# Kernel optimization log

Hardware: AMD Instinct MI355X
Metric: run time of the kernel (lower is better)

Reference implementation:

```python
import jax, jax.numpy as jnp
import numpy as np

N, E = 50000, 500000
G_DIM, H1, H2 = 256, 128, 128
N_REL, N_BASES = 8, 30  # 2 * n_speakers**2 with n_speakers=2


def setup_inputs() -> dict:
    key = jax.random.key(0)
    ks = jax.random.split(key, 12)
    inp = {
        "node_features": jax.random.normal(ks[0], (N, G_DIM), jnp.float32),
        "edge_index": jax.random.randint(ks[1], (2, E), 0, N, jnp.int64),
        "edge_norm": jax.random.uniform(ks[2], (E,), jnp.float32),
        "edge_type": jax.random.randint(ks[3], (E,), 0, N_REL, jnp.int64),
        # RGCNConv (basis decomposition) params
        "basis": jax.random.normal(ks[4], (N_BASES, G_DIM, H1), jnp.float32) / np.sqrt(G_DIM),
        "comp": jax.random.normal(ks[5], (N_REL, N_BASES), jnp.float32) / np.sqrt(N_BASES),
        "root": jax.random.normal(ks[6], (G_DIM, H1), jnp.float32) / np.sqrt(G_DIM),
        "bias1": jnp.zeros((H1,), jnp.float32),
        # GATv2Conv params (heads=1)
        "w_l": jax.random.normal(ks[7], (H1, H2), jnp.float32) / np.sqrt(H1),
        "w_r": jax.random.normal(ks[8], (H1, H2), jnp.float32) / np.sqrt(H1),
        "att": jax.random.normal(ks[9], (H2,), jnp.float32) / np.sqrt(H2),
        "bias2": jnp.zeros((H2,), jnp.float32),
    }
    return inp


def reference(node_features, edge_index, edge_norm, edge_type,
              basis, comp, root, bias1, w_l, w_r, att, bias2):
    # NOTE: edge_norm is accepted but unused, matching the original forward.
    src, dst = edge_index[0], edge_index[1]
    n = node_features.shape[0]
    R = comp.shape[0]

    # ---- RGCNConv with basis decomposition, per-relation mean aggregation ----
    Wr = jnp.einsum('rb,bio->rio', comp, basis)            # [R, g_dim, h1]
    xr = jnp.einsum('ni,rio->nro', node_features, Wr)      # [N, R, h1]
    msg = xr[src, edge_type]                               # [E, h1] gather per edge
    seg = dst * R + edge_type                              # segment = (node, relation)
    sums = jax.ops.segment_sum(msg, seg, num_segments=n * R)
    cnts = jax.ops.segment_sum(jnp.ones((msg.shape[0],), msg.dtype), seg, num_segments=n * R)
    mean = sums / jnp.maximum(cnts, 1.0)[:, None]          # per-(node,relation) mean
    agg = mean.reshape(n, R, -1).sum(axis=1)               # sum over relations
    x1 = agg + node_features @ root + bias1                # [N, h1]

    # ---- GATv2Conv (heads=1, add_self_loops=True) ----
    loop = jnp.arange(n, dtype=src.dtype)
    s2 = jnp.concatenate([src, loop])
    d2 = jnp.concatenate([dst, loop])
    xl = x1 @ w_l                                          # source transform [N, h2]
    xrt = x1 @ w_r                                         # target transform [N, h2]
    e = jax.nn.leaky_relu(xl[s2] + xrt[d2], 0.2) @ att     # [E+N] edge scores
    emax = jax.ops.segment_max(e, d2, num_segments=n)      # self-loops => every seg nonempty
    ex = jnp.exp(e - emax[d2])
    denom = jax.ops.segment_sum(ex, d2, num_segments=n)
    alpha = ex / denom[d2]                                 # segment softmax over incoming edges
    out = jax.ops.segment_sum(alpha[:, None] * xl[s2], d2, num_segments=n) + bias2
    return out
```

## Files before the change

kernel.cpp:

```cpp
#include <hip/hip_runtime.h>
#include <hip/hip_bf16.h>
#include <cstdint>
#include <cstddef>

#define NN 50000
#define NE 500000
#define GD 256
#define H1 128
#define H2 128
#define NREL 8
#define NBASES 30
#define XRLD (NREL * H1)
#define NCHUNKS ((NN + 1023) / 1024)

typedef __attribute__((ext_vector_type(8))) short bf16x8;
typedef __attribute__((ext_vector_type(4))) float f32x4;
typedef __attribute__((ext_vector_type(8))) unsigned short u16x8;
typedef __attribute__((ext_vector_type(4))) unsigned int u32x4;

__device__ __forceinline__ float lrelu(float x) { return x > 0.f ? x : 0.2f * x; }

__device__ __forceinline__ unsigned short f2bf(float x) {
  union { float f; uint32_t u; } v; v.f = x;
  uint32_t r = v.u + 0x7FFF + ((v.u >> 16) & 1);
  return (unsigned short)(r >> 16);
}
__device__ __forceinline__ float bf2f(unsigned short u) {
  union { uint32_t u; float f; } v; v.u = ((uint32_t)u) << 16;
  return v.f;
}

template <int N>
__device__ __forceinline__ void wait_vmcnt() {
  asm volatile("s_waitcnt vmcnt(%0)" :: "n"(N) : "memory");
}

__device__ __forceinline__ void gload_lds(const unsigned short* gp, unsigned short* lp) {
  __builtin_amdgcn_global_load_lds(
      (const __attribute__((address_space(1))) void*)gp,
      (__attribute__((address_space(3))) void*)lp, 16, 0, 0);
}

__global__ void k_cast(const float* __restrict__ in, unsigned short* __restrict__ out) {
  int i = blockIdx.x * 256 + threadIdx.x;
  const float4* p = (const float4*)(in + (size_t)i * 8);
  float4 a = p[0], b = p[1];
  u16x8 r;
  r[0] = f2bf(a.x); r[1] = f2bf(a.y); r[2] = f2bf(a.z); r[3] = f2bf(a.w);
  r[4] = f2bf(b.x); r[5] = f2bf(b.y); r[6] = f2bf(b.z); r[7] = f2bf(b.w);
  *(u16x8*)(out + (size_t)i * 8) = r;
}

__global__ void k_wr(const float* __restrict__ basis, const float* __restrict__ comp,
                     unsigned short* __restrict__ wrb_t) {
  int idx = blockIdx.x * 256 + threadIdx.x;
  int n = idx >> 8;
  int k = idx & 255;
  int r = n >> 7, o = n & 127;
  float acc = 0.f;
  #pragma unroll
  for (int b = 0; b < NBASES; b++)
    acc += comp[r * NBASES + b] * basis[((size_t)b * GD + k) * H1 + o];
  wrb_t[idx] = f2bf(acc);
}

__global__ __launch_bounds__(256)
void k_prep2(const float* __restrict__ root, const float* __restrict__ w_l,
             const float* __restrict__ w_r, const float* __restrict__ bias1,
             unsigned short* __restrict__ btf, float* __restrict__ biasv) {
  __shared__ float wcol[128];
  __shared__ float red[128];
  int c = blockIdx.x;
  int t = threadIdx.x;
  if (t < 128) {
    float v = (c < H2) ? w_l[t * H2 + c] : w_r[t * H2 + (c - H2)];
    wcol[t] = v;
    btf[c * 384 + t] = f2bf(v);
  }
  __syncthreads();
  const float4* rp = (const float4*)(root + (size_t)t * H1);
  float acc = 0.f;
  #pragma unroll
  for (int j4 = 0; j4 < 32; j4++) {
    float4 r4 = rp[j4];
    acc += r4.x * wcol[j4 * 4 + 0] + r4.y * wcol[j4 * 4 + 1] +
           r4.z * wcol[j4 * 4 + 2] + r4.w * wcol[j4 * 4 + 3];
  }
  btf[c * 384 + 128 + t] = f2bf(acc);
  if (t < 128) red[t] = bias1[t] * wcol[t];
  __syncthreads();
  for (int st = 64; st > 0; st >>= 1) {
    if (t < st) red[t] += red[t + st];
    __syncthreads();
  }
  if (t == 0) biasv[c] = red[0];
}

template <int K, int WM>
__global__ __launch_bounds__(256, 3)
void k_mgemm(const unsigned short* __restrict__ A, const unsigned short* __restrict__ Bt,
             unsigned short* __restrict__ C, int M, int N, int gx) {
  constexpr int BM = WM * 32;
  constexpr int ACH = BM * 4;
  constexpr int TCH = ACH + 512;
  constexpr int LPT = TCH / 256;
  constexpr int NS = K / 32;
  constexpr int ABUF = BM * 32;
  constexpr int BBUF = 128 * 32;
  extern __shared__ unsigned short lds[];
  const int tid = threadIdx.x;
  const int lane = tid & 63;
  const int wave = tid >> 6;

  const int nwg = gridDim.x;
  const int q = nwg >> 3, r = nwg & 7;
  const int xcd = blockIdx.x & 7, bi = blockIdx.x >> 3;
  const int wg = (xcd < r ? xcd * (q + 1) : r * (q + 1) + (xcd - r) * q) + bi;
  const int bx = wg % gx;
  const int by = wg / gx;
  const int row0 = by * BM;
  const int colb = bx * 128;
  const int wcol = (wave & 1) * 64;
  const int wrow = (wave >> 1) * (WM * 16);
  const int lr = lane & 15;
  const int lko = lane >> 4;

  f32x4 acc[WM][4];
  #pragma unroll
  for (int i = 0; i < WM; i++)
    #pragma unroll
    for (int j = 0; j < 4; j++) acc[i][j] = (f32x4){0.f, 0.f, 0.f, 0.f};

  auto stage = [&](int k0, int b) {
    unsigned short* as = lds + b * ABUF;
    unsigned short* bs = lds + 3 * ABUF + b * BBUF;
    #pragma unroll
    for (int it = 0; it < LPT; it++) {
      int ci = it * 256 + tid;
      if (ci < ACH) {
        int row = ci >> 2, cs = ci & 3;
        int s = (row & 3) ^ ((row >> 2) & 3);
        int gm = row0 + row; if (gm >= M) gm = M - 1;
        gload_lds(A + (size_t)gm * K + k0 + ((cs ^ s) << 3), as + (size_t)ci * 8);
      } else {
        int cj = ci - ACH;
        int row = cj >> 2, cs = cj & 3;
        int s = (row & 3) ^ ((row >> 2) & 3);
        gload_lds(Bt + (size_t)(colb + row) * K + k0 + ((cs ^ s) << 3), bs + (size_t)cj * 8);
      }
    }
  };

  auto compute = [&](int b) {
    const unsigned short* as = lds + b * ABUF;
    const unsigned short* bs = lds + 3 * ABUF + b * BBUF;
    bf16x8 af[WM], bfr[4];
    #pragma unroll
    for (int mb = 0; mb < WM; mb++) {
      int rowL = wrow + mb * 16 + lr;
      int s = (rowL & 3) ^ ((rowL >> 2) & 3);
      af[mb] = *(const bf16x8*)&as[rowL * 32 + ((lko ^ s) << 3)];
    }
    #pragma unroll
    for (int nb = 0; nb < 4; nb++) {
      int colL = wcol + nb * 16 + lr;
      int s = (colL & 3) ^ ((colL >> 2) & 3);
      bfr[nb] = *(const bf16x8*)&bs[colL * 32 + ((lko ^ s) << 3)];
    }
    #pragma unroll
    for (int mb = 0; mb < WM; mb++)
      #pragma unroll
      for (int nb = 0; nb < 4; nb++)
        acc[mb][nb] = __builtin_amdgcn_mfma_f32_16x16x32_bf16(af[mb], bfr[nb], acc[mb][nb], 0, 0, 0);
  };

  stage(0, 0);
  stage(32, 1);
  wait_vmcnt<LPT>();
  __builtin_amdgcn_sched_barrier(0);
  __builtin_amdgcn_s_barrier();
  #pragma unroll
  for (int s = 0; s < NS; s++) {
    if (s + 2 < NS) stage((s + 2) * 32, (s + 2) % 3);
    compute(s % 3);
    if (s + 1 < NS) {
      if (s + 2 < NS) wait_vmcnt<LPT>();
      else            wait_vmcnt<0>();
      __builtin_amdgcn_sched_barrier(0);
      __builtin_amdgcn_s_barrier();
    }
  }

  __syncthreads();
  unsigned short* Cs = lds;
  const int orow = lko * 4;
  #pragma unroll
  for (int mb = 0; mb < WM; mb++) {
    #pragma unroll
    for (int i = 0; i < 4; i++) {
      int row = wrow + mb * 16 + orow + i;
      int sw = (row & 7) << 3;
      #pragma unroll
      for (int nb = 0; nb < 4; nb++) {
        int col = wcol + nb * 16 + lr;
        Cs[row * 128 + (col ^ sw)] = f2bf(acc[mb][nb][i]);
      }
    }
  }
  __syncthreads();
  #pragma unroll
  for (int it = 0; it < BM / 16; it++) {
    int off = it * 256 + tid;
    int row = off >> 4, jb = off & 15;
    int grow = row0 + row;
    if (grow < M) {
      int idx = row * 128 + ((jb * 8) ^ ((row & 7) << 3));
      u32x4 val = *(const u32x4*)&Cs[idx];
      __builtin_nontemporal_store(val, (u32x4*)&C[(size_t)grow * N + colb + jb * 8]);
    }
  }
}

__global__ __launch_bounds__(256, 3)
void k_fused(const unsigned short* __restrict__ A1, const unsigned short* __restrict__ A2,
             const unsigned short* __restrict__ Bt, const float* __restrict__ biasv,
             unsigned short* __restrict__ xl, unsigned short* __restrict__ xrt, int M) {
  constexpr int K = 384, NS = 12, LPT = 4;
  extern __shared__ unsigned short lds[];
  const int tid = threadIdx.x;
  const int lane = tid & 63;
  const int wave = tid >> 6;

  const int nwg = gridDim.x;
  const int q = nwg >> 3, r = nwg & 7;
  const int xcd = blockIdx.x & 7, bi = blockIdx.x >> 3;
  const int wg = (xcd < r ? xcd * (q + 1) : r * (q + 1) + (xcd - r) * q) + bi;
  const int bx = wg & 1;
  const int by = wg >> 1;
  const int row0 = by * 128;
  const int colb = bx * 128;
  const int wcol = (wave & 1) * 64;
  const int wrow = (wave >> 1) * 64;
  const int lr = lane & 15;
  const int lko = lane >> 4;

  f32x4 acc[4][4];
  #pragma unroll
  for (int i = 0; i < 4; i++)
    #pragma unroll
    for (int j = 0; j < 4; j++) acc[i][j] = (f32x4){0.f, 0.f, 0.f, 0.f};

  auto stage = [&](int k0, int b) {
    unsigned short* as = lds + b * 4096;
    unsigned short* bs = lds + 3 * 4096 + b * 4096;
    #pragma unroll
    for (int it = 0; it < LPT; it++) {
      int ci = it * 256 + tid;
      if (ci < 512) {
        int row = ci >> 2, cs = ci & 3;
        int s = (row & 3) ^ ((row >> 2) & 3);
        int gm = row0 + row; if (gm >= M) gm = M - 1;
        const unsigned short* gp;
        if (k0 < 128) gp = A1 + (size_t)gm * 128 + k0 + ((cs ^ s) << 3);
        else          gp = A2 + (size_t)gm * 256 + (k0 - 128) + ((cs ^ s) << 3);
        gload_lds(gp, as + (size_t)ci * 8);
      } else {
        int cj = ci - 512;
        int row = cj >> 2, cs = cj & 3;
        int s = (row & 3) ^ ((row >> 2) & 3);
        gload_lds(Bt + (size_t)(colb + row) * K + k0 + ((cs ^ s) << 3), bs + (size_t)cj * 8);
      }
    }
  };

  auto compute = [&](int b) {
    const unsigned short* as = lds + b * 4096;
    const unsigned short* bs = lds + 3 * 4096 + b * 4096;
    bf16x8 af[4], bfr[4];
    #pragma unroll
    for (int mb = 0; mb < 4; mb++) {
      int rowL = wrow + mb * 16 + lr;
      int s = (rowL & 3) ^ ((rowL >> 2) & 3);
      af[mb] = *(const bf16x8*)&as[rowL * 32 + ((lko ^ s) << 3)];
    }
    #pragma unroll
    for (int nb = 0; nb < 4; nb++) {
      int colL = wcol + nb * 16 + lr;
      int s = (colL & 3) ^ ((colL >> 2) & 3);
      bfr[nb] = *(const bf16x8*)&bs[colL * 32 + ((lko ^ s) << 3)];
    }
    #pragma unroll
    for (int mb = 0; mb < 4; mb++)
      #pragma unroll
      for (int nb = 0; nb < 4; nb++)
        acc[mb][nb] = __builtin_amdgcn_mfma_f32_16x16x32_bf16(af[mb], bfr[nb], acc[mb][nb], 0, 0, 0);
  };

  stage(0, 0);
  stage(32, 1);
  wait_vmcnt<LPT>();
  __builtin_amdgcn_sched_barrier(0);
  __builtin_amdgcn_s_barrier();
  #pragma unroll
  for (int s = 0; s < NS; s++) {
    if (s + 2 < NS) stage((s + 2) * 32, (s + 2) % 3);
    compute(s % 3);
    if (s + 1 < NS) {
      if (s + 2 < NS) wait_vmcnt<LPT>();
      else            wait_vmcnt<0>();
      __builtin_amdgcn_sched_barrier(0);
      __builtin_amdgcn_s_barrier();
    }
  }

  __syncthreads();
  unsigned short* Cs = lds;
  const int orow = lko * 4;
  #pragma unroll
  for (int mb = 0; mb < 4; mb++) {
    #pragma unroll
    for (int i = 0; i < 4; i++) {
      int row = wrow + mb * 16 + orow + i;
      int sw = (row & 7) << 3;
      #pragma unroll
      for (int nb = 0; nb < 4; nb++) {
        int col = wcol + nb * 16 + lr;
        Cs[row * 128 + (col ^ sw)] = f2bf(acc[mb][nb][i] + biasv[colb + col]);
      }
    }
  }
  __syncthreads();
  unsigned short* Cout = bx ? xrt : xl;
  #pragma unroll
  for (int it = 0; it < 8; it++) {
    int off = it * 256 + tid;
    int row = off >> 4, jb = off & 15;
    int grow = row0 + row;
    if (grow < M) {
      int idx = row * 128 + ((jb * 8) ^ ((row & 7) << 3));
      *(u16x8*)&Cout[(size_t)grow * 128 + jb * 8] = *(const u16x8*)&Cs[idx];
    }
  }
}

__global__ void k_deg(const int* __restrict__ ei, const int* __restrict__ et,
                      int* __restrict__ cnt2) {
  int e = blockIdx.x * 256 + threadIdx.x;
  if (e < NE) atomicAdd(&cnt2[ei[NE + e] * NREL + et[e]], 1);
}

__device__ __forceinline__ int node_deg(const int* cnt2, int n) {
  const int4* p = (const int4*)(cnt2 + n * NREL);
  int4 a = p[0], b = p[1];
  return a.x + a.y + a.z + a.w + b.x + b.y + b.z + b.w;
}

__global__ void k_scan_a(const int* __restrict__ cnt2, int* __restrict__ parts) {
  __shared__ int lds[256];
  int t = threadIdx.x;
  int base = blockIdx.x * 1024 + t * 4;
  int s = 0;
  #pragma unroll
  for (int j = 0; j < 4; j++) s += (base + j < NN) ? node_deg(cnt2, base + j) : 0;
  lds[t] = s;
  __syncthreads();
  for (int st = 128; st > 0; st >>= 1) {
    if (t < st) lds[t] += lds[t + st];
    __syncthreads();
  }
  if (t == 0) parts[blockIdx.x] = lds[0];
}

__global__ void k_scan_b(int* __restrict__ parts) {
  int t = threadIdx.x;
  int v = (t < NCHUNKS) ? parts[t] : 0;
  int x = v;
  #pragma unroll
  for (int off = 1; off < 64; off <<= 1) {
    int y = __shfl_up(x, off, 64);
    if (t >= off) x += y;
  }
  if (t < NCHUNKS) parts[t] = x - v;
}

__global__ void k_scan_c(const int* __restrict__ cnt2, const int* __restrict__ parts,
                         int* __restrict__ rowptr) {
  __shared__ int lds[256];
  int t = threadIdx.x;
  int base = blockIdx.x * 1024 + t * 4;
  int v[4];
  int s = 0;
  #pragma unroll
  for (int j = 0; j < 4; j++) { v[j] = (base + j < NN) ? node_deg(cnt2, base + j) : 0; s += v[j]; }
  lds[t] = s;
  __syncthreads();
  for (int st = 1; st < 256; st <<= 1) {
    int add = (t >= st) ? lds[t - st] : 0;
    __syncthreads();
    lds[t] += add;
    __syncthreads();
  }
  int excl = lds[t] - s;
  int off = parts[blockIdx.x];
  int run = 0;
  #pragma unroll
  for (int j = 0; j < 4; j++) {
    run += v[j];
    if (base + j < NN) rowptr[base + j + 1] = off + excl + run;
  }
  if (blockIdx.x == 0 && t == 0) rowptr[0] = 0;
}

__global__ void k_scatter(const int* __restrict__ ei, const int* __restrict__ et,
                          const int* __restrict__ rowptr, const int* __restrict__ cnt2,
                          int* __restrict__ cursor, int* __restrict__ csr,
                          float* __restrict__ wgt) {
  int e = blockIdx.x * 256 + threadIdx.x;
  if (e < NE) {
    int d = ei[NE + e];
    int r = et[e];
    int pos = atomicAdd(&cursor[d], 1);
    int slot = rowptr[d] + pos;
    csr[slot] = ei[e] | (r << 20);
    wgt[slot] = 1.0f / (float)cnt2[d * NREL + r];
  }
}

__global__ __launch_bounds__(256)
void k_rgcn(const unsigned short* __restrict__ xr, const int* __restrict__ csr2,
            const float* __restrict__ wgt, const int* __restrict__ rowptr,
            unsigned short* __restrict__ agg) {
  int wpair = (blockIdx.x * 256 + threadIdx.x) >> 6;
  int lane = threadIdx.x & 63;
  int hb = lane & 32;
  int l = lane & 31;
  int wid = wpair * 2 + (hb >> 5);
  if (wid >= NN) return;
  int c0 = l * 4;
  float a0 = 0.f, a1 = 0.f, a2 = 0.f, a3 = 0.f;
  int beg = rowptr[wid], end = rowptr[wid + 1];
  for (int j0 = beg; j0 < end; j0 += 32) {
    int nv = end - j0; if (nv > 32) nv = 32;
    int pk = (l < nv) ? csr2[j0 + l] : 0;
    float wk = (l < nv) ? wgt[j0 + l] : 0.f;
    for (int t = 0; t < nv; t += 8) {
      uint2 wv[8]; float wz[8];
      #pragma unroll
      for (int z = 0; z < 8; z++) {
        int p = __shfl(pk, hb + t + z, 64);
        wz[z] = __shfl(wk, hb + t + z, 64);
        if (t + z < nv) {
          size_t off = (size_t)(p & 0xFFFFF) * XRLD + (p >> 20) * H1 + c0;
          wv[z] = *(const uint2*)(xr + off);
        } else {
          wv[z] = make_uint2(0, 0);
        }
      }
      #pragma unroll
      for (int z = 0; z < 8; z++) {
        a0 += wz[z] * bf2f((unsigned short)(wv[z].x & 0xffff));
        a1 += wz[z] * bf2f((unsigned short)(wv[z].x >> 16));
        a2 += wz[z] * bf2f((unsigned short)(wv[z].y & 0xffff));
        a3 += wz[z] * bf2f((unsigned short)(wv[z].y >> 16));
      }
    }
  }
  uint2 packed;
  packed.x = (uint32_t)f2bf(a0) | ((uint32_t)f2bf(a1) << 16);
  packed.y = (uint32_t)f2bf(a2) | ((uint32_t)f2bf(a3) << 16);
  *(uint2*)&agg[(size_t)wid * H1 + c0] = packed;
}

__global__ __launch_bounds__(256)
void k_gat(const unsigned short* __restrict__ xl, const unsigned short* __restrict__ xrt,
           const int* __restrict__ csr2, const int* __restrict__ rowptr,
           const float* __restrict__ att, const float* __restrict__ bias2,
           float* __restrict__ out) {
  int wpair = (blockIdx.x * 256 + threadIdx.x) >> 6;
  int lane = threadIdx.x & 63;
  int hb = lane & 32;
  int l = lane & 31;
  int wid = wpair * 2 + (hb >> 5);
  if (wid >= NN) return;
  int c0 = l * 4;
  float4 at = *(const float4*)(att + c0);
  uint2 wr2 = *(const uint2*)(xrt + (size_t)wid * 128 + c0);
  float xr0 = bf2f((unsigned short)(wr2.x & 0xffff));
  float xr1 = bf2f((unsigned short)(wr2.x >> 16));
  float xr2 = bf2f((unsigned short)(wr2.y & 0xffff));
  float xr3 = bf2f((unsigned short)(wr2.y >> 16));
  uint2 wv0 = *(const uint2*)(xl + (size_t)wid * 128 + c0);
  float v0 = bf2f((unsigned short)(wv0.x & 0xffff));
  float v1 = bf2f((unsigned short)(wv0.x >> 16));
  float v2 = bf2f((unsigned short)(wv0.y & 0xffff));
  float v3 = bf2f((unsigned short)(wv0.y >> 16));
  float ep = lrelu(v0 + xr0) * at.x + lrelu(v1 + xr1) * at.y +
             lrelu(v2 + xr2) * at.z + lrelu(v3 + xr3) * at.w;
  #pragma unroll
  for (int off = 16; off > 0; off >>= 1) ep += __shfl_xor(ep, off, 64);
  float m = ep, s = 1.f, o0 = v0, o1 = v1, o2 = v2, o3 = v3;
  int beg = rowptr[wid], end = rowptr[wid + 1];
  for (int j0 = beg; j0 < end; j0 += 32) {
    int nv = end - j0; if (nv > 32) nv = 32;
    int pk = (l < nv) ? csr2[j0 + l] : 0;
    for (int t = 0; t < nv; t += 8) {
      float u0[8], u1[8], u2[8], u3[8], p[8];
      #pragma unroll
      for (int z = 0; z < 8; z++) {
        int src = __shfl(pk, hb + t + z, 64) & 0xFFFFF;
        uint2 wu;
        if (t + z < nv) wu = *(const uint2*)(xl + (size_t)src * 128 + c0);
        else            wu = make_uint2(0, 0);
        u0[z] = bf2f((unsigned short)(wu.x & 0xffff));
        u1[z] = bf2f((unsigned short)(wu.x >> 16));
        u2[z] = bf2f((unsigned short)(wu.y & 0xffff));
        u3[z] = bf2f((unsigned short)(wu.y >> 16));
      }
      #pragma unroll
      for (int z = 0; z < 8; z++)
        p[z] = lrelu(u0[z] + xr0) * at.x + lrelu(u1[z] + xr1) * at.y +
               lrelu(u2[z] + xr2) * at.z + lrelu(u3[z] + xr3) * at.w;
      #pragma unroll
      for (int off = 16; off > 0; off >>= 1) {
        #pragma unroll
        for (int z = 0; z < 8; z++) p[z] += __shfl_xor(p[z], off, 64);
      }
      #pragma unroll
      for (int z = 0; z < 8; z++) if (t + z >= nv) p[z] = -1e30f;
      float pm = p[0];
      #pragma unroll
      for (int z = 1; z < 8; z++) pm = fmaxf(pm, p[z]);
      float mn = fmaxf(m, pm);
      float sc = __expf(m - mn);
      float e[8];
      #pragma unroll
      for (int z = 0; z < 8; z++) e[z] = __expf(p[z] - mn);
      float es = 0.f, e0 = 0.f, e1 = 0.f, e2 = 0.f, e3 = 0.f;
      #pragma unroll
      for (int z = 0; z < 8; z++) {
        es += e[z]; e0 += e[z] * u0[z]; e1 += e[z] * u1[z];
        e2 += e[z] * u2[z]; e3 += e[z] * u3[z];
      }
      s = s * sc + es;
      o0 = o0 * sc + e0; o1 = o1 * sc + e1;
      o2 = o2 * sc + e2; o3 = o3 * sc + e3;
      m = mn;
    }
  }
  float inv = 1.f / s;
  float4 b2 = *(const float4*)(bias2 + c0);
  float4 res = make_float4(o0 * inv + b2.x, o1 * inv + b2.y,
                           o2 * inv + b2.z, o3 * inv + b2.w);
  *(float4*)&out[(size_t)wid * H1 + c0] = res;
}

extern "C" void kernel_launch(void* const* d_in, const int* in_sizes, int n_in,
                              void* d_out, int out_size, void* d_ws, size_t ws_size,
                              hipStream_t stream) {
  const float* nf    = (const float*)d_in[0];
  const int*   ei    = (const int*)d_in[1];
  const int*   et    = (const int*)d_in[3];
  const float* basis = (const float*)d_in[4];
  const float* comp  = (const float*)d_in[5];
  const float* root  = (const float*)d_in[6];
  const float* bias1 = (const float*)d_in[7];
  const float* w_l   = (const float*)d_in[8];
  const float* w_r   = (const float*)d_in[9];
  const float* att   = (const float*)d_in[10];
  const float* bias2 = (const float*)d_in[11];
  float* out = (float*)d_out;

  char* ws = (char*)d_ws;
  unsigned short* xr_bf  = (unsigned short*)ws;
  unsigned short* nf_bf  = (unsigned short*)(ws + 102400000);
  unsigned short* wrb_t  = (unsigned short*)(ws + 128000000);
  unsigned short* btf    = (unsigned short*)(ws + 128524288);
  float*          biasv  = (float*)(ws + 128720896);
  unsigned short* agg_bf = (unsigned short*)(ws + 128721920);
  int*            cursor = (int*)(ws + 141521920);
  int*            cnt2   = cursor + NN;
  int*            rowptr = cnt2 + NN * NREL;
  int*            csr    = rowptr + NN + 1;
  int*            parts  = csr + NE;
  float*          wgt    = (float*)(parts + 64);
  unsigned short* xl_bf  = (unsigned short*)ws;
  unsigned short* xrt_bf = (unsigned short*)(ws + 12800000);

  hipMemsetAsync(cursor, 0, (1 + NREL) * NN * sizeof(int), stream);

  k_cast<<<(NN * GD / 8) / 256, 256, 0, stream>>>(nf, nf_bf);
  k_wr<<<(XRLD * GD) / 256, 256, 0, stream>>>(basis, comp, wrb_t);
  k_prep2<<<256, 256, 0, stream>>>(root, w_l, w_r, bias1, btf, biasv);

  const int GY128 = (NN + 127) / 128;
  k_mgemm<256, 4><<<8 * GY128, 256, 49152, stream>>>(
      nf_bf, wrb_t, xr_bf, NN, XRLD, 8);

  k_deg<<<(NE + 255) / 256, 256, 0, stream>>>(ei, et, cnt2);
  k_scan_a<<<NCHUNKS, 256, 0, stream>>>(cnt2, parts);
  k_scan_b<<<1, 64, 0, stream>>>(parts);
  k_scan_c<<<NCHUNKS, 256, 0, stream>>>(cnt2, parts, rowptr);
  k_scatter<<<(NE + 255) / 256, 256, 0, stream>>>(ei, et, rowptr, cnt2, cursor, csr, wgt);

  k_rgcn<<<(NN + 7) / 8, 256, 0, stream>>>(xr_bf, csr, wgt, rowptr, agg_bf);

  k_fused<<<2 * GY128, 256, 49152, stream>>>(agg_bf, nf_bf, btf, biasv, xl_bf, xrt_bf, NN);

  k_gat<<<(NN + 7) / 8, 256, 0, stream>>>(xl_bf, xrt_bf, csr, rowptr, att, bias2, out);
}
```

Before: 241.3 us.

## Merge prep kernels, fold scan offsets into scan_c, pack counts into CSR

Three preprocessing launches (bf16 cast, relation-weight build, root/W fold) become one kernel that branches on block index. The single-block scan of chunk partial sums is folded into each scan_c block, which removes one tiny serial launch. The per-edge mean weight array is dropped: the per-(node,relation) count is packed into the upper bits of the CSR word, and the RGCN gather takes its reciprocal on the fly. This saves launch gaps and the writing and reading of a separate weight array. In exchange the node index is limited to 16 bits and the count to 13 bits, and each scan_c block now repeats the partials scan.

```diff
diff --git a/kernel.cpp b/kernel.cpp
--- a/kernel.cpp
+++ b/kernel.cpp
@@ -41,59 +41,63 @@
       (__attribute__((address_space(3))) void*)lp, 16, 0, 0);
 }
 
-__global__ void k_cast(const float* __restrict__ in, unsigned short* __restrict__ out) {
-  int i = blockIdx.x * 256 + threadIdx.x;
-  const float4* p = (const float4*)(in + (size_t)i * 8);
-  float4 a = p[0], b = p[1];
-  u16x8 r;
-  r[0] = f2bf(a.x); r[1] = f2bf(a.y); r[2] = f2bf(a.z); r[3] = f2bf(a.w);
-  r[4] = f2bf(b.x); r[5] = f2bf(b.y); r[6] = f2bf(b.z); r[7] = f2bf(b.w);
-  *(u16x8*)(out + (size_t)i * 8) = r;
-}
-
-__global__ void k_wr(const float* __restrict__ basis, const float* __restrict__ comp,
-                     unsigned short* __restrict__ wrb_t) {
-  int idx = blockIdx.x * 256 + threadIdx.x;
-  int n = idx >> 8;
-  int k = idx & 255;
-  int r = n >> 7, o = n & 127;
-  float acc = 0.f;
-  #pragma unroll
-  for (int b = 0; b < NBASES; b++)
-    acc += comp[r * NBASES + b] * basis[((size_t)b * GD + k) * H1 + o];
-  wrb_t[idx] = f2bf(acc);
-}
-
+#define PRE_CAST_BLKS 6250
+#define PRE_WR_BLKS   1024
+#define PRE_ALL_BLKS  (PRE_CAST_BLKS + PRE_WR_BLKS + 256)
 __global__ __launch_bounds__(256)
-void k_prep2(const float* __restrict__ root, const float* __restrict__ w_l,
-             const float* __restrict__ w_r, const float* __restrict__ bias1,
-             unsigned short* __restrict__ btf, float* __restrict__ biasv) {
+void k_pre3(const float* __restrict__ nf, unsigned short* __restrict__ nf_bf,
+            const float* __restrict__ basis, const float* __restrict__ comp,
+            unsigned short* __restrict__ wrb_t,
+            const float* __restrict__ root, const float* __restrict__ w_l,
+            const float* __restrict__ w_r, const float* __restrict__ bias1,
+            unsigned short* __restrict__ btf, float* __restrict__ biasv) {
   __shared__ float wcol[128];
   __shared__ float red[128];
-  int c = blockIdx.x;
-  int t = threadIdx.x;
-  if (t < 128) {
-    float v = (c < H2) ? w_l[t * H2 + c] : w_r[t * H2 + (c - H2)];
-    wcol[t] = v;
-    btf[c * 384 + t] = f2bf(v);
-  }
-  __syncthreads();
-  const float4* rp = (const float4*)(root + (size_t)t * H1);
-  float acc = 0.f;
-  #pragma unroll
-  for (int j4 = 0; j4 < 32; j4++) {
-    float4 r4 = rp[j4];
-    acc += r4.x * wcol[j4 * 4 + 0] + r4.y * wcol[j4 * 4 + 1] +
-           r4.z * wcol[j4 * 4 + 2] + r4.w * wcol[j4 * 4 + 3];
-  }
-  btf[c * 384 + 128 + t] = f2bf(acc);
-  if (t < 128) red[t] = bias1[t] * wcol[t];
-  __syncthreads();
-  for (int st = 64; st > 0; st >>= 1) {
-    if (t < st) red[t] += red[t + st];
+  const int b = blockIdx.x;
+  const int t = threadIdx.x;
+  if (b < PRE_CAST_BLKS) {
+    int i = b * 256 + t;
+    const float4* p = (const float4*)(nf + (size_t)i * 8);
+    float4 a = p[0], bb = p[1];
+    u16x8 r;
+    r[0] = f2bf(a.x); r[1] = f2bf(a.y); r[2] = f2bf(a.z); r[3] = f2bf(a.w);
+    r[4] = f2bf(bb.x); r[5] = f2bf(bb.y); r[6] = f2bf(bb.z); r[7] = f2bf(bb.w);
+    *(u16x8*)(nf_bf + (size_t)i * 8) = r;
+  } else if (b < PRE_CAST_BLKS + PRE_WR_BLKS) {
+    int idx = (b - PRE_CAST_BLKS) * 256 + t;
+    int n = idx >> 8;
+    int k = idx & 255;
+    int r = n >> 7, o = n & 127;
+    float acc = 0.f;
+    #pragma unroll
+    for (int bs = 0; bs < NBASES; bs++)
+      acc += comp[r * NBASES + bs] * basis[((size_t)bs * GD + k) * H1 + o];
+    wrb_t[idx] = f2bf(acc);
+  } else {
+    int c = b - (PRE_CAST_BLKS + PRE_WR_BLKS);
+    if (t < 128) {
+      float v = (c < H2) ? w_l[t * H2 + c] : w_r[t * H2 + (c - H2)];
+      wcol[t] = v;
+      btf[c * 384 + t] = f2bf(v);
+    }
     __syncthreads();
-  }
-  if (t == 0) biasv[c] = red[0];
+    const float4* rp = (const float4*)(root + (size_t)t * H1);
+    float acc = 0.f;
+    #pragma unroll
+    for (int j4 = 0; j4 < 32; j4++) {
+      float4 r4 = rp[j4];
+      acc += r4.x * wcol[j4 * 4 + 0] + r4.y * wcol[j4 * 4 + 1] +
+             r4.z * wcol[j4 * 4 + 2] + r4.w * wcol[j4 * 4 + 3];
+    }
+    btf[c * 384 + 128 + t] = f2bf(acc);
+    if (t < 128) red[t] = bias1[t] * wcol[t];
+    __syncthreads();
+    for (int st = 64; st > 0; st >>= 1) {
+      if (t < st) red[t] += red[t + st];
+      __syncthreads();
+    }
+    if (t == 0) biasv[c] = red[0];
+  }
 }
 
 template <int K, int WM>
@@ -371,22 +375,21 @@
   if (t == 0) parts[blockIdx.x] = lds[0];
 }
 
-__global__ void k_scan_b(int* __restrict__ parts) {
-  int t = threadIdx.x;
-  int v = (t < NCHUNKS) ? parts[t] : 0;
-  int x = v;
-  #pragma unroll
-  for (int off = 1; off < 64; off <<= 1) {
-    int y = __shfl_up(x, off, 64);
-    if (t >= off) x += y;
-  }
-  if (t < NCHUNKS) parts[t] = x - v;
-}
-
 __global__ void k_scan_c(const int* __restrict__ cnt2, const int* __restrict__ parts,
                          int* __restrict__ rowptr) {
   __shared__ int lds[256];
+  __shared__ int blkoff;
   int t = threadIdx.x;
+  if (t < 64) {
+    int v = (t < NCHUNKS) ? parts[t] : 0;
+    int x = v;
+    #pragma unroll
+    for (int off = 1; off < 64; off <<= 1) {
+      int y = __shfl_up(x, off, 64);
+      if (t >= off) x += y;
+    }
+    if (t == (int)blockIdx.x) blkoff = x - v;
+  }
   int base = blockIdx.x * 1024 + t * 4;
   int v[4];
   int s = 0;
@@ -401,7 +404,7 @@
     __syncthreads();
   }
   int excl = lds[t] - s;
-  int off = parts[blockIdx.x];
+  int off = blkoff;
   int run = 0;
   #pragma unroll
   for (int j = 0; j < 4; j++) {
@@ -413,23 +416,20 @@
 
 __global__ void k_scatter(const int* __restrict__ ei, const int* __restrict__ et,
                           const int* __restrict__ rowptr, const int* __restrict__ cnt2,
-                          int* __restrict__ cursor, int* __restrict__ csr,
-                          float* __restrict__ wgt) {
+                          int* __restrict__ cursor, unsigned int* __restrict__ csr) {
   int e = blockIdx.x * 256 + threadIdx.x;
   if (e < NE) {
     int d = ei[NE + e];
     int r = et[e];
     int pos = atomicAdd(&cursor[d], 1);
-    int slot = rowptr[d] + pos;
-    csr[slot] = ei[e] | (r << 20);
-    wgt[slot] = 1.0f / (float)cnt2[d * NREL + r];
+    unsigned int cnt = (unsigned int)cnt2[d * NREL + r];
+    csr[rowptr[d] + pos] = (unsigned int)ei[e] | ((unsigned int)r << 16) | (cnt << 19);
   }
 }
 
 __global__ __launch_bounds__(256)
-void k_rgcn(const unsigned short* __restrict__ xr, const int* __restrict__ csr2,
-            const float* __restrict__ wgt, const int* __restrict__ rowptr,
-            unsigned short* __restrict__ agg) {
+void k_rgcn(const unsigned short* __restrict__ xr, const unsigned int* __restrict__ csr2,
+            const int* __restrict__ rowptr, unsigned short* __restrict__ agg) {
   int wpair = (blockIdx.x * 256 + threadIdx.x) >> 6;
   int lane = threadIdx.x & 63;
   int hb = lane & 32;
@@ -441,19 +441,19 @@
   int beg = rowptr[wid], end = rowptr[wid + 1];
   for (int j0 = beg; j0 < end; j0 += 32) {
     int nv = end - j0; if (nv > 32) nv = 32;
-    int pk = (l < nv) ? csr2[j0 + l] : 0;
-    float wk = (l < nv) ? wgt[j0 + l] : 0.f;
+    unsigned int pk = (l < nv) ? csr2[j0 + l] : 0u;
     for (int t = 0; t < nv; t += 8) {
       uint2 wv[8]; float wz[8];
       #pragma unroll
       for (int z = 0; z < 8; z++) {
-        int p = __shfl(pk, hb + t + z, 64);
-        wz[z] = __shfl(wk, hb + t + z, 64);
+        unsigned int p = (unsigned int)__shfl((int)pk, hb + t + z, 64);
         if (t + z < nv) {
-          size_t off = (size_t)(p & 0xFFFFF) * XRLD + (p >> 20) * H1 + c0;
+          size_t off = (size_t)(p & 0xFFFF) * XRLD + ((p >> 16) & 7) * H1 + c0;
           wv[z] = *(const uint2*)(xr + off);
+          wz[z] = __builtin_amdgcn_rcpf((float)(p >> 19));
         } else {
           wv[z] = make_uint2(0, 0);
+          wz[z] = 0.f;
         }
       }
       #pragma unroll
@@ -473,7 +473,7 @@
 
 __global__ __launch_bounds__(256)
 void k_gat(const unsigned short* __restrict__ xl, const unsigned short* __restrict__ xrt,
-           const int* __restrict__ csr2, const int* __restrict__ rowptr,
+           const unsigned int* __restrict__ csr2, const int* __restrict__ rowptr,
            const float* __restrict__ att, const float* __restrict__ bias2,
            float* __restrict__ out) {
   int wpair = (blockIdx.x * 256 + threadIdx.x) >> 6;
@@ -502,12 +502,13 @@
   int beg = rowptr[wid], end = rowptr[wid + 1];
   for (int j0 = beg; j0 < end; j0 += 32) {
     int nv = end - j0; if (nv > 32) nv = 32;
-    int pk = (l < nv) ? csr2[j0 + l] : 0;
+    unsigned int pk = (l < nv) ? csr2[j0 + l] : 0u;
     for (int t = 0; t < nv; t += 8) {
       float u0[8], u1[8], u2[8], u3[8], p[8];
       #pragma unroll
       for (int z = 0; z < 8; z++) {
-        int src = __shfl(pk, hb + t + z, 64) & 0xFFFFF;
+        unsigned int pv = (unsigned int)__shfl((int)pk, hb + t + z, 64);
+        int src = (int)(pv & 0xFFFF);
         uint2 wu;
         if (t + z < nv) wu = *(const uint2*)(xl + (size_t)src * 128 + c0);
         else            wu = make_uint2(0, 0);
@@ -580,17 +581,15 @@
   int*            cursor = (int*)(ws + 141521920);
   int*            cnt2   = cursor + NN;
   int*            rowptr = cnt2 + NN * NREL;
-  int*            csr    = rowptr + NN + 1;
-  int*            parts  = csr + NE;
-  float*          wgt    = (float*)(parts + 64);
+  unsigned int*   csr    = (unsigned int*)(rowptr + NN + 1);
+  int*            parts  = (int*)(csr + NE);
   unsigned short* xl_bf  = (unsigned short*)ws;
   unsigned short* xrt_bf = (unsigned short*)(ws + 12800000);
 
   hipMemsetAsync(cursor, 0, (1 + NREL) * NN * sizeof(int), stream);
 
-  k_cast<<<(NN * GD / 8) / 256, 256, 0, stream>>>(nf, nf_bf);
-  k_wr<<<(XRLD * GD) / 256, 256, 0, stream>>>(basis, comp, wrb_t);
-  k_prep2<<<256, 256, 0, stream>>>(root, w_l, w_r, bias1, btf, biasv);
+  k_pre3<<<PRE_ALL_BLKS, 256, 0, stream>>>(nf, nf_bf, basis, comp, wrb_t,
+                                           root, w_l, w_r, bias1, btf, biasv);
 
   const int GY128 = (NN + 127) / 128;
   k_mgemm<256, 4><<<8 * GY128, 256, 49152, stream>>>(
@@ -598,11 +597,10 @@
 
   k_deg<<<(NE + 255) / 256, 256, 0, stream>>>(ei, et, cnt2);
   k_scan_a<<<NCHUNKS, 256, 0, stream>>>(cnt2, parts);
-  k_scan_b<<<1, 64, 0, stream>>>(parts);
   k_scan_c<<<NCHUNKS, 256, 0, stream>>>(cnt2, parts, rowptr);
-  k_scatter<<<(NE + 255) / 256, 256, 0, stream>>>(ei, et, rowptr, cnt2, cursor, csr, wgt);
-
-  k_rgcn<<<(NN + 7) / 8, 256, 0, stream>>>(xr_bf, csr, wgt, rowptr, agg_bf);
+  k_scatter<<<(NE + 255) / 256, 256, 0, stream>>>(ei, et, rowptr, cnt2, cursor, csr);
+
+  k_rgcn<<<(NN + 7) / 8, 256, 0, stream>>>(xr_bf, csr, rowptr, agg_bf);
 
   k_fused<<<2 * GY128, 256, 49152, stream>>>(agg_bf, nf_bf, btf, biasv, xl_bf, xrt_bf, NN);
 
```

Result: no change. 240.6 us (-0.3%).
